# Kernel tuning notes

Hardware: AMD Instinct MI355X
Metric: run time of the kernel (lower is better)

## Reference

```python
import jax, jax.numpy as jnp
import numpy as np

NUM_TAGS = 5
START_TAG = 3  # ent_to_ix['<START>']
STOP_TAG = 4   # ent_to_ix['<STOP>']
NEG_INF = -10000.0
B, T = 8192, 512


def setup_inputs() -> dict:
    key = jax.random.key(0)
    k1, k2 = jax.random.split(key)
    feats = jax.random.normal(k1, (B, T, NUM_TAGS), dtype=jnp.float32)
    transitions = jax.random.normal(k2, (NUM_TAGS, NUM_TAGS), dtype=jnp.float32)
    # matches __init__: no transition into START, none out of STOP
    transitions = transitions.at[START_TAG, :].set(NEG_INF)
    transitions = transitions.at[:, STOP_TAG].set(NEG_INF)
    return {"feats": feats, "transitions": transitions}


def reference(feats, transitions):
    """Batched CRF forward algorithm (log partition function).

    feats: [B, T, K] emission scores; transitions: [K, K] where
    transitions[next, prev] is the score of prev -> next.
    Returns alpha: [B] log partition per sequence.
    """
    def single(seq):  # seq: [T, K]
        init = jnp.full((NUM_TAGS,), NEG_INF, dtype=seq.dtype).at[START_TAG].set(0.0)

        def step(forward_var, feat):
            # scores[next, prev] = forward_var[prev] + transitions[next, prev] + feat[next]
            scores = forward_var[None, :] + transitions + feat[:, None]
            return jax.nn.logsumexp(scores, axis=1), None

        forward_var, _ = jax.lax.scan(step, init, seq)
        terminal = forward_var + transitions[STOP_TAG]
        return jax.nn.logsumexp(terminal)

    return jax.vmap(single)(feats)
```

## Files before the change

### kernel.cpp

```cpp
#include <hip/hip_runtime.h>

#define BB 8192
#define SEQF 2560

typedef float v2f __attribute__((ext_vector_type(2)));

__device__ __forceinline__ float rfl(float x) {
    return __int_as_float(__builtin_amdgcn_readfirstlane(__float_as_int(x)));
}
__device__ __forceinline__ v2f vsplat(float x) { return (v2f){x, x}; }

__global__ __launch_bounds__(128, 4) void crf_fused(const float* __restrict__ feats,
                                                    const float* __restrict__ trans,
                                                    float* __restrict__ out) {
    const int tid  = threadIdx.x;
    const int lane = tid & 63;
    const int half = lane >> 5;
    const int cpos = lane & 31;
    const int wv   = tid >> 6;
    const int s0   = (blockIdx.x * 2 + wv) * 2;

    const float4* p = (const float4*)(feats + (size_t)(s0 + half) * SEQF) + cpos * 20;
    float4 q0 =p[0],  q1 =p[1],  q2 =p[2],  q3 =p[3],  q4 =p[4];
    float4 q5 =p[5],  q6 =p[6],  q7 =p[7],  q8 =p[8],  q9 =p[9];
    float4 q10=p[10], q11=p[11], q12=p[12], q13=p[13], q14=p[14];
    float4 q15=p[15], q16=p[16], q17=p[17], q18=p[18], q19=p[19];
    __builtin_amdgcn_sched_barrier(0);

    const float BIAS = 0.13533528323661270f;
    const float E00=rfl(__expf(trans[0])*BIAS),  E01=rfl(__expf(trans[1])*BIAS),  E02=rfl(__expf(trans[2])*BIAS);
    const float E10=rfl(__expf(trans[5])*BIAS),  E11=rfl(__expf(trans[6])*BIAS),  E12=rfl(__expf(trans[7])*BIAS);
    const float E20=rfl(__expf(trans[10])*BIAS), E21=rfl(__expf(trans[11])*BIAS), E22=rfl(__expf(trans[12])*BIAS);
    const float C0 =rfl(__expf(trans[3])*BIAS),  C1 =rfl(__expf(trans[8])*BIAS),  C2 =rfl(__expf(trans[13])*BIAS);
    const float S0 =rfl(__expf(trans[20])), S1 =rfl(__expf(trans[21])), S2 =rfl(__expf(trans[22]));

    const v2f E00p=vsplat(E00), E01p=vsplat(E01), E02p=vsplat(E02);
    const v2f E10p=vsplat(E10), E11p=vsplat(E11), E12p=vsplat(E12);
    const v2f E20p=vsplat(E20), E21p=vsplat(E21), E22p=vsplat(E22);

    const bool c0 = (cpos == 0);
    const v2f GA0 = c0 ? vsplat(C0) : (v2f){E00, E01};
    const v2f GA1 = c0 ? vsplat(C1) : (v2f){E10, E11};
    const v2f GA2 = c0 ? vsplat(C2) : (v2f){E20, E21};
    const float GB0 = c0 ? C0 : E02;
    const float GB1 = c0 ? C1 : E12;
    const float GB2 = c0 ? C2 : E22;

    v2f MA0, MA1, MA2;
    float MB0, MB1, MB2;
    float ls = 0.0f;

#define CRF_STEP(FA, FB, FC) do {                                   \
        float e0 = __expf(FA), e1 = __expf(FB), e2 = __expf(FC);    \
        v2f NA0 = vsplat(e0) * (E00p*MA0 + E01p*MA1 + E02p*MA2);    \
        v2f NA1 = vsplat(e1) * (E10p*MA0 + E11p*MA1 + E12p*MA2);    \
        v2f NA2 = vsplat(e2) * (E20p*MA0 + E21p*MA1 + E22p*MA2);    \
        float NB0 = e0 * (E00*MB0 + E01*MB1 + E02*MB2);             \
        float NB1 = e1 * (E10*MB0 + E11*MB1 + E12*MB2);             \
        float NB2 = e2 * (E20*MB0 + E21*MB1 + E22*MB2);             \
        MA0=NA0; MA1=NA1; MA2=NA2; MB0=NB0; MB1=NB1; MB2=NB2;       \
    } while (0)

#define CRF_RENORM() do {                                           \
        v2f mp = __builtin_elementwise_max(__builtin_elementwise_max(MA0, MA1), MA2); \
        float mm = fmaxf(fmaxf(mp.x, mp.y), fmaxf(fmaxf(MB0, MB1), MB2)); \
        mm = fmaxf(mm, 1e-30f);                                     \
        int ee = (int)((__float_as_uint(mm) >> 23) & 0xffu) - 127;  \
        float sc = __uint_as_float((unsigned)(127 - ee) << 23);     \
        ls += (float)ee;                                            \
        v2f scp = vsplat(sc);                                       \
        MA0*=scp; MA1*=scp; MA2*=scp; MB0*=sc; MB1*=sc; MB2*=sc;    \
    } while (0)

#define TREE_LEVEL(D, RN) do {                                      \
        v2f PA0, PA1, PA2;                                          \
        PA0.x=__shfl_down(MA0.x,D); PA0.y=__shfl_down(MA0.y,D);     \
        PA1.x=__shfl_down(MA1.x,D); PA1.y=__shfl_down(MA1.y,D);     \
        PA2.x=__shfl_down(MA2.x,D); PA2.y=__shfl_down(MA2.y,D);     \
        float PB0=__shfl_down(MB0,D), PB1=__shfl_down(MB1,D), PB2=__shfl_down(MB2,D); \
        float Pls=__shfl_down(ls, D);                               \
        v2f NA0 = vsplat(PA0.x)*MA0 + vsplat(PA0.y)*MA1 + vsplat(PB0)*MA2; \
        v2f NA1 = vsplat(PA1.x)*MA0 + vsplat(PA1.y)*MA1 + vsplat(PB1)*MA2; \
        v2f NA2 = vsplat(PA2.x)*MA0 + vsplat(PA2.y)*MA1 + vsplat(PB2)*MA2; \
        float NB0 = PA0.x*MB0 + PA0.y*MB1 + PB0*MB2;                \
        float NB1 = PA1.x*MB0 + PA1.y*MB1 + PB1*MB2;                \
        float NB2 = PA2.x*MB0 + PA2.y*MB1 + PB2*MB2;                \
        MA0=NA0; MA1=NA1; MA2=NA2; MB0=NB0; MB1=NB1; MB2=NB2;       \
        ls += Pls;                                                  \
        if (RN) CRF_RENORM();                                       \
    } while (0)

    {
        float e0 = __expf(q0.x), e1 = __expf(q0.y), e2 = __expf(q0.z);
        MA0 = vsplat(e0) * GA0;  MB0 = e0 * GB0;
        MA1 = vsplat(e1) * GA1;  MB1 = e1 * GB1;
        MA2 = vsplat(e2) * GA2;  MB2 = e2 * GB2;
    }
    CRF_STEP(q1.y,  q1.z,  q1.w);
    CRF_STEP(q2.z,  q2.w,  q3.x);
    CRF_STEP(q3.w,  q4.x,  q4.y);
    CRF_STEP(q5.x,  q5.y,  q5.z);
    CRF_STEP(q6.y,  q6.z,  q6.w);
    CRF_STEP(q7.z,  q7.w,  q8.x);
    CRF_STEP(q8.w,  q9.x,  q9.y);
    CRF_STEP(q10.x, q10.y, q10.z);
    CRF_STEP(q11.y, q11.z, q11.w);
    CRF_STEP(q12.z, q12.w, q13.x);
    CRF_STEP(q13.w, q14.x, q14.y);
    CRF_STEP(q15.x, q15.y, q15.z);
    CRF_STEP(q16.y, q16.z, q16.w);
    CRF_STEP(q17.z, q17.w, q18.x);
    CRF_STEP(q18.w, q19.x, q19.y);
    CRF_RENORM();

    TREE_LEVEL(1, 0);
    TREE_LEVEL(2, 0);
    TREE_LEVEL(4, 1);
    TREE_LEVEL(8, 0);
    TREE_LEVEL(16, 1);

    float r = S0*MA0.x + S1*MA1.x + S2*MA2.x;
    float res = __logf(r) + ls * 0.69314718055994531f + 1024.0f;
    if (cpos == 0) out[s0 + half] = res;

#undef CRF_STEP
#undef CRF_RENORM
#undef TREE_LEVEL
}

extern "C" void kernel_launch(void* const* d_in, const int* in_sizes, int n_in,
                              void* d_out, int out_size, void* d_ws, size_t ws_size,
                              hipStream_t stream) {
    const float* feats = (const float*)d_in[0];
    const float* trans = (const float*)d_in[1];
    float* out = (float*)d_out;
    (void)d_ws; (void)ws_size;

    crf_fused<<<BB / 4, 128, 0, stream>>>(feats, trans, out);
}
```

Baseline: 19.59 us.

## Coalesce feature loads with lane-pair interleave and shuffle redistribution

Lanes now load feature vectors in an interleaved pattern, so adjacent lanes read adjacent 16-byte chunks across the two sequences, instead of each lane reading a contiguous 320-byte block. The loaded values are then swapped between lane pairs with xor-shuffles and selects, so each lane ends up with its original chunk of the sequence. The goal is better coalescing of global loads, at the cost of 40 extra shuffles per lane and higher register pressure. Launch bounds are relaxed from 4 to 3 waves per SIMD to leave room for the extra registers.

```diff
diff --git a/kernel.cpp b/kernel.cpp
--- a/kernel.cpp
+++ b/kernel.cpp
@@ -10,21 +10,34 @@
 }
 __device__ __forceinline__ v2f vsplat(float x) { return (v2f){x, x}; }
 
-__global__ __launch_bounds__(128, 4) void crf_fused(const float* __restrict__ feats,
+__device__ __forceinline__ float4 shfl4x1(float4 v) {
+    float4 r;
+    r.x = __shfl_xor(v.x, 1); r.y = __shfl_xor(v.y, 1);
+    r.z = __shfl_xor(v.z, 1); r.w = __shfl_xor(v.w, 1);
+    return r;
+}
+__device__ __forceinline__ float4 sel4(int c, float4 a, float4 b) {
+    return make_float4(c ? a.x : b.x, c ? a.y : b.y, c ? a.z : b.z, c ? a.w : b.w);
+}
+
+__global__ __launch_bounds__(128, 3) void crf_fused(const float* __restrict__ feats,
                                                     const float* __restrict__ trans,
                                                     float* __restrict__ out) {
     const int tid  = threadIdx.x;
     const int lane = tid & 63;
     const int half = lane >> 5;
     const int cpos = lane & 31;
+    const int b    = lane & 1;
+    const int p    = lane >> 1;
     const int wv   = tid >> 6;
     const int s0   = (blockIdx.x * 2 + wv) * 2;
 
-    const float4* p = (const float4*)(feats + (size_t)(s0 + half) * SEQF) + cpos * 20;
-    float4 q0 =p[0],  q1 =p[1],  q2 =p[2],  q3 =p[3],  q4 =p[4];
-    float4 q5 =p[5],  q6 =p[6],  q7 =p[7],  q8 =p[8],  q9 =p[9];
-    float4 q10=p[10], q11=p[11], q12=p[12], q13=p[13], q14=p[14];
-    float4 q15=p[15], q16=p[16], q17=p[17], q18=p[18], q19=p[19];
+    const float4* base = (const float4*)(feats + (size_t)s0 * SEQF);
+    float4 r0 =base[p*40+ 0+b], r1 =base[p*40+ 2+b], r2 =base[p*40+ 4+b], r3 =base[p*40+ 6+b];
+    float4 r4 =base[p*40+ 8+b], r5 =base[p*40+10+b], r6 =base[p*40+12+b], r7 =base[p*40+14+b];
+    float4 r8 =base[p*40+16+b], r9 =base[p*40+18+b], r10=base[p*40+20+b], r11=base[p*40+22+b];
+    float4 r12=base[p*40+24+b], r13=base[p*40+26+b], r14=base[p*40+28+b], r15=base[p*40+30+b];
+    float4 r16=base[p*40+32+b], r17=base[p*40+34+b], r18=base[p*40+36+b], r19=base[p*40+38+b];
     __builtin_amdgcn_sched_barrier(0);
 
     const float BIAS = 0.13533528323661270f;
@@ -37,6 +50,19 @@
     const v2f E00p=vsplat(E00), E01p=vsplat(E01), E02p=vsplat(E02);
     const v2f E10p=vsplat(E10), E11p=vsplat(E11), E12p=vsplat(E12);
     const v2f E20p=vsplat(E20), E21p=vsplat(E21), E22p=vsplat(E22);
+
+    float4 q[20];
+#define REDIST(i, RLO, RHI) do {                        \
+        float4 te = shfl4x1(RLO);                       \
+        float4 to = shfl4x1(RHI);                       \
+        q[2*(i)]   = sel4(b, to, RLO);                  \
+        q[2*(i)+1] = sel4(b, RHI, te);                  \
+    } while (0)
+    REDIST(0, r0, r10); REDIST(1, r1, r11); REDIST(2, r2, r12);
+    REDIST(3, r3, r13); REDIST(4, r4, r14); REDIST(5, r5, r15);
+    REDIST(6, r6, r16); REDIST(7, r7, r17); REDIST(8, r8, r18);
+    REDIST(9, r9, r19);
+#undef REDIST
 
     const bool c0 = (cpos == 0);
     const v2f GA0 = c0 ? vsplat(C0) : (v2f){E00, E01};
@@ -91,26 +117,26 @@
     } while (0)
 
     {
-        float e0 = __expf(q0.x), e1 = __expf(q0.y), e2 = __expf(q0.z);
+        float e0 = __expf(q[0].x), e1 = __expf(q[0].y), e2 = __expf(q[0].z);
         MA0 = vsplat(e0) * GA0;  MB0 = e0 * GB0;
         MA1 = vsplat(e1) * GA1;  MB1 = e1 * GB1;
         MA2 = vsplat(e2) * GA2;  MB2 = e2 * GB2;
     }
-    CRF_STEP(q1.y,  q1.z,  q1.w);
-    CRF_STEP(q2.z,  q2.w,  q3.x);
-    CRF_STEP(q3.w,  q4.x,  q4.y);
-    CRF_STEP(q5.x,  q5.y,  q5.z);
-    CRF_STEP(q6.y,  q6.z,  q6.w);
-    CRF_STEP(q7.z,  q7.w,  q8.x);
-    CRF_STEP(q8.w,  q9.x,  q9.y);
-    CRF_STEP(q10.x, q10.y, q10.z);
-    CRF_STEP(q11.y, q11.z, q11.w);
-    CRF_STEP(q12.z, q12.w, q13.x);
-    CRF_STEP(q13.w, q14.x, q14.y);
-    CRF_STEP(q15.x, q15.y, q15.z);
-    CRF_STEP(q16.y, q16.z, q16.w);
-    CRF_STEP(q17.z, q17.w, q18.x);
-    CRF_STEP(q18.w, q19.x, q19.y);
+    CRF_STEP(q[1].y,  q[1].z,  q[1].w);
+    CRF_STEP(q[2].z,  q[2].w,  q[3].x);
+    CRF_STEP(q[3].w,  q[4].x,  q[4].y);
+    CRF_STEP(q[5].x,  q[5].y,  q[5].z);
+    CRF_STEP(q[6].y,  q[6].z,  q[6].w);
+    CRF_STEP(q[7].z,  q[7].w,  q[8].x);
+    CRF_STEP(q[8].w,  q[9].x,  q[9].y);
+    CRF_STEP(q[10].x, q[10].y, q[10].z);
+    CRF_STEP(q[11].y, q[11].z, q[11].w);
+    CRF_STEP(q[12].z, q[12].w, q[13].x);
+    CRF_STEP(q[13].w, q[14].x, q[14].y);
+    CRF_STEP(q[15].x, q[15].y, q[15].z);
+    CRF_STEP(q[16].y, q[16].z, q[16].w);
+    CRF_STEP(q[17].z, q[17].w, q[18].x);
+    CRF_STEP(q[18].w, q[19].x, q[19].y);
     CRF_RENORM();
 
     TREE_LEVEL(1, 0);
```

After: 19.96 us. About the same (+1.9%).
